# Kernel tuning notes

Hardware: AMD Instinct MI355X
Metric: run time of the kernel (lower is better)

The kernel has to match this reference:

```python
import jax, jax.numpy as jnp
import numpy as np
import math

B, T, D = 2, 2048, 1024
H, DH = 16, 64  # n_heads, d_head
ROPE_THETA = 10000.0


def _rope_cos_sin(seq_len, d_head, dtype):
    # inv_freq over even indices, freqs[i,j] = t_i * inv_freq_j, shape [T, d_head//2]
    inv_freq = 1.0 / (ROPE_THETA ** (jnp.arange(0, d_head, 2, dtype=jnp.float32) / d_head))
    freqs = jnp.arange(seq_len, dtype=jnp.float32)[:, None] * inv_freq[None, :]
    # emb = cat(freqs, freqs); we only ever index cos[..., :d_head//2], so keep the half
    cos = jnp.cos(freqs).astype(dtype)[None, :, None, :]  # [1,T,1,DH/2]
    sin = jnp.sin(freqs).astype(dtype)[None, :, None, :]
    return cos, sin


def _apply_rotation(x, cos, sin):
    # x: [B,T,H,DH]; rotate-half style as in the torch module
    x1, x2 = x[..., : x.shape[-1] // 2], x[..., x.shape[-1] // 2 :]
    return jnp.concatenate([x1 * cos - x2 * sin, x1 * sin + x2 * cos], axis=-1)


def setup_inputs() -> dict:
    key = jax.random.key(0)
    k1, k2, k3 = jax.random.split(key, 3)
    x = jax.random.normal(k1, (B, T, D), dtype=jnp.float32)
    # torch Linear weights stored transposed here as [in, out]; init_std=0.02
    Wqkv = jax.random.normal(k2, (D, 3 * D), dtype=jnp.float32) * 0.02
    Wout = jax.random.normal(k3, (D, D), dtype=jnp.float32) * 0.02
    return {"x": x, "Wqkv": Wqkv, "Wout": Wout}


def reference(x, Wqkv, Wout):
    b, t, d = x.shape
    qkv = x @ Wqkv  # [B,T,3D]
    q, k, v = jnp.split(qkv, 3, axis=-1)
    q = q.reshape(b, t, H, DH)
    k = k.reshape(b, t, H, DH)
    v = v.reshape(b, t, H, DH)

    cos, sin = _rope_cos_sin(t, DH, x.dtype)
    q = _apply_rotation(q, cos, sin)
    k = _apply_rotation(k, cos, sin)

    scale = 1.0 / math.sqrt(DH)
    # scores: [B,H,Tq,Tk]
    scores = jnp.einsum("bqhd,bkhd->bhqk", q, k) * scale
    causal = jnp.triu(jnp.ones((t, t), dtype=bool), k=1)
    scores = jnp.where(causal[None, None, :, :], -jnp.inf, scores)
    attn = jax.nn.softmax(scores, axis=-1)
    # dropout in eval mode -> identity
    out = jnp.einsum("bhqk,bkhd->bqhd", attn, v).reshape(b, t, d)
    return out @ Wout
```

## Files before the change

### kernel.cpp

```cpp
#include <hip/hip_runtime.h>
#include <hip/hip_bf16.h>
#include <stdint.h>
#include <math.h>

#define T_SEQ 2048
#define NHEAD 16
#define NBH   32
#define BTROW 4096

typedef __bf16 bf16_t;
typedef __bf16 bf16x4_t __attribute__((ext_vector_type(4)));
typedef __bf16 bf16x8_t __attribute__((ext_vector_type(8)));
typedef float  f32x4_t  __attribute__((ext_vector_type(4)));

#define QSCALE 0.18033688011112042f

__device__ __forceinline__ f32x4_t mfma16(bf16x8_t a, bf16x8_t b, f32x4_t c) {
  return __builtin_amdgcn_mfma_f32_16x16x32_bf16(a, b, c, 0, 0, 0);
}

__device__ __forceinline__ float fast_exp2(float x) {
#if __has_builtin(__builtin_amdgcn_exp2f)
  return __builtin_amdgcn_exp2f(x);
#else
  return exp2f(x);
#endif
}

__device__ __forceinline__ void gl_lds16(const bf16_t* g, bf16_t* l) {
  __builtin_amdgcn_global_load_lds(
      (const __attribute__((address_space(1))) void*)g,
      (__attribute__((address_space(3))) void*)l, 16, 0, 0);
}

__global__ __launch_bounds__(256) void k_cast_bf16(const float* __restrict__ in,
                                                   bf16_t* __restrict__ out, int n) {
  int tid = blockIdx.x * blockDim.x + threadIdx.x;
  int stride = gridDim.x * blockDim.x;
  for (int i = tid * 4; i < n; i += stride * 4) {
    float4 a = *(const float4*)(in + i);
    bf16x4_t r = { (bf16_t)a.x, (bf16_t)a.y, (bf16_t)a.z, (bf16_t)a.w };
    *(bf16x4_t*)(out + i) = r;
  }
}

__global__ __launch_bounds__(256) void k_trans_cast(const float* __restrict__ W,
                                                    bf16_t* __restrict__ WT,
                                                    int K, int N) {
  __shared__ float tile[32][33];
  int n0 = blockIdx.x * 32, k0 = blockIdx.y * 32;
  int tx = threadIdx.x & 31, ty = threadIdx.x >> 5;
#pragma unroll
  for (int j = 0; j < 4; j++)
    tile[ty + j * 8][tx] = W[(size_t)(k0 + ty + j * 8) * N + n0 + tx];
  __syncthreads();
#pragma unroll
  for (int j = 0; j < 4; j++)
    WT[(size_t)(n0 + ty + j * 8) * K + k0 + tx] = (bf16_t)tile[tx][ty + j * 8];
}

__global__ __launch_bounds__(256) void k_rope_table(float* __restrict__ cs,
                                                    float* __restrict__ sn) {
  int i = blockIdx.x * blockDim.x + threadIdx.x;
  if (i >= T_SEQ * 32) return;
  int t = i >> 5, j = i & 31;
  float inv = powf(10000.0f, -(float)(2 * j) / 64.0f);
  float f = (float)t * inv;
  cs[i] = cosf(f);
  sn[i] = sinf(f);
}

__global__ __launch_bounds__(256) void k_gemm_qkv(const bf16_t* __restrict__ A,
                                                  const bf16_t* __restrict__ Bt,
                                                  const float* __restrict__ cs,
                                                  const float* __restrict__ sn,
                                                  bf16_t* __restrict__ Qr,
                                                  bf16_t* __restrict__ Kr,
                                                  bf16_t* __restrict__ Vt) {
  const int K = 1024;
  __shared__ __align__(16) unsigned char smem[33792];
  bf16_t* vtile = (bf16_t*)smem;

  int m0 = blockIdx.y * 128, n0 = blockIdx.x * 128;
  int tid = threadIdx.x;
  int lane = tid & 63, w = tid >> 6;
  int wr = w >> 1, wc = w & 1;
  int l15 = lane & 15, l4 = lane >> 4;

  f32x4_t acc[4][4];
#pragma unroll
  for (int m = 0; m < 4; m++)
#pragma unroll
    for (int n = 0; n < 4; n++) acc[m][n] = (f32x4_t){0.f, 0.f, 0.f, 0.f};

  auto stageg = [&](int bf, int k0) {
    bf16_t* As = (bf16_t*)(smem + bf * 16384);
    bf16_t* Bs = (bf16_t*)(smem + 8192 + bf * 16384);
#pragma unroll
    for (int j = 0; j < 2; j++) {
      int c = j * 256 + tid;
      int row = c >> 2, kb = c & 3;
      gl_lds16(A + (size_t)(m0 + row) * K + k0 + kb * 8, As + (size_t)(j * 256 + w * 64) * 8);
      gl_lds16(Bt + (size_t)(n0 + row) * K + k0 + kb * 8, Bs + (size_t)(j * 256 + w * 64) * 8);
    }
  };

  stageg(0, 0);
  for (int kt = 0; kt < 32; kt++) {
    int cb = kt & 1;
    bf16_t* As = (bf16_t*)(smem + cb * 16384);
    bf16_t* Bs = (bf16_t*)(smem + 8192 + cb * 16384);
    asm volatile("s_waitcnt vmcnt(0)" ::: "memory");
    __builtin_amdgcn_s_barrier();
    if (kt + 1 < 32) stageg(cb ^ 1, (kt + 1) * 32);
    bf16x8_t af[4], bfr[4];
#pragma unroll
    for (int m = 0; m < 4; m++)
      af[m] = *(const bf16x8_t*)(As + (size_t)(wr * 64 + m * 16 + l15) * 32 + l4 * 8);
#pragma unroll
    for (int n = 0; n < 4; n++)
      bfr[n] = *(const bf16x8_t*)(Bs + (size_t)(wc * 64 + n * 16 + l15) * 32 + l4 * 8);
#pragma unroll
    for (int m = 0; m < 4; m++)
#pragma unroll
      for (int n = 0; n < 4; n++) acc[m][n] = mfma16(af[m], bfr[n], acc[m][n]);
  }
  __syncthreads();

  int region = n0 >> 10;
  if (region < 2) {
    bf16_t* dst = region ? Kr : Qr;
    float qs = region ? 1.0f : QSCALE;
    int h = ((n0 & 1023) + wc * 64) >> 6;
#pragma unroll
    for (int m = 0; m < 4; m++)
#pragma unroll
      for (int r = 0; r < 4; r++) {
        int row = m0 + wr * 64 + m * 16 + l4 * 4 + r;
        int b = row >> 11, t = row & 2047;
        size_t obase = ((size_t)(b * NHEAD + h) * T_SEQ + t) * 64;
#pragma unroll
        for (int n = 0; n < 2; n++) {
          int j = n * 16 + l15;
          float c = cs[t * 32 + j], s = sn[t * 32 + j];
          float x1 = acc[m][n][r], x2 = acc[m][n + 2][r];
          dst[obase + j]      = (bf16_t)((x1 * c - x2 * s) * qs);
          dst[obase + 32 + j] = (bf16_t)((x1 * s + x2 * c) * qs);
        }
      }
  } else {
#pragma unroll
    for (int m = 0; m < 4; m++)
#pragma unroll
      for (int n = 0; n < 4; n++)
#pragma unroll
        for (int r = 0; r < 4; r++)
          vtile[(size_t)(wc * 64 + n * 16 + l15) * 132 + wr * 64 + m * 16 + l4 * 4 + r] =
              (bf16_t)acc[m][n][r];
    __syncthreads();
    int colbase = n0 - 2048;
    int b = m0 >> 11, t0l = m0 & 2047;
#pragma unroll
    for (int p = 0; p < 64; p++) {
      int idx = p * 256 + tid;
      int dl = idx >> 7, tl = idx & 127;
      int col = colbase + dl, h = col >> 6, d = col & 63;
      Vt[((size_t)(b * NHEAD + h) * 64 + d) * T_SEQ + t0l + tl] = vtile[(size_t)dl * 132 + tl];
    }
  }
}

__global__ __launch_bounds__(256) void k_gemm2(const bf16_t* __restrict__ A,
                                               const bf16_t* __restrict__ Bt,
                                               float* __restrict__ C) {
  const int N = 1024, K = 1024;
  __shared__ __align__(16) bf16_t As[2][64 * 32];
  __shared__ __align__(16) bf16_t Bs[2][128 * 32];
  int m0 = blockIdx.y * 64, n0 = blockIdx.x * 128;
  int tid = threadIdx.x;
  int lane = tid & 63, w = tid >> 6;
  int l15 = lane & 15, l4 = lane >> 4;

  f32x4_t acc[4][2];
#pragma unroll
  for (int m = 0; m < 4; m++)
#pragma unroll
    for (int n = 0; n < 2; n++) acc[m][n] = (f32x4_t){0.f, 0.f, 0.f, 0.f};

  auto stageg = [&](int bf, int k0) {
    {
      int row = tid >> 2, kb = tid & 3;
      gl_lds16(A + (size_t)(m0 + row) * K + k0 + kb * 8, &As[bf][0] + (size_t)(w * 64) * 8);
    }
#pragma unroll
    for (int j = 0; j < 2; j++) {
      int c = j * 256 + tid;
      int row = c >> 2, kb = c & 3;
      gl_lds16(Bt + (size_t)(n0 + row) * K + k0 + kb * 8, &Bs[bf][0] + (size_t)(j * 256 + w * 64) * 8);
    }
  };

  stageg(0, 0);
  for (int kt = 0; kt < 32; kt++) {
    int cb = kt & 1;
    asm volatile("s_waitcnt vmcnt(0)" ::: "memory");
    __builtin_amdgcn_s_barrier();
    if (kt + 1 < 32) stageg(cb ^ 1, (kt + 1) * 32);
    bf16x8_t af[4], bfr[2];
#pragma unroll
    for (int m = 0; m < 4; m++)
      af[m] = *(const bf16x8_t*)(&As[cb][0] + (size_t)(m * 16 + l15) * 32 + l4 * 8);
#pragma unroll
    for (int n = 0; n < 2; n++)
      bfr[n] = *(const bf16x8_t*)(&Bs[cb][0] + (size_t)(w * 32 + n * 16 + l15) * 32 + l4 * 8);
#pragma unroll
    for (int m = 0; m < 4; m++)
#pragma unroll
      for (int n = 0; n < 2; n++) acc[m][n] = mfma16(af[m], bfr[n], acc[m][n]);
  }
#pragma unroll
  for (int m = 0; m < 4; m++)
#pragma unroll
    for (int n = 0; n < 2; n++)
#pragma unroll
      for (int r = 0; r < 4; r++) {
        int row = m0 + m * 16 + l4 * 4 + r;
        int col = n0 + w * 32 + n * 16 + l15;
        C[(size_t)row * N + col] = acc[m][n][r];
      }
}

__global__ __launch_bounds__(512, 4) void k_attn(const bf16_t* __restrict__ Qr,
                                                 const bf16_t* __restrict__ Kr,
                                                 const bf16_t* __restrict__ Vt,
                                                 bf16_t* __restrict__ Ob) {
  __shared__ __align__(16) bf16_t Ks[2][2][64 * 64];
  __shared__ __align__(16) bf16_t Vs[2][2][64 * 64];
  __shared__ __align__(16) bf16_t Ps[8][16 * 64];
  int flat = blockIdx.x;
  int swz = (flat & 7) * 64 + (flat >> 3);
  int pair = swz & 15, bh = swz >> 4;
  int b = bh >> 4, h = bh & 15;
  int tid = threadIdx.x, lane = tid & 63, w = tid >> 6;
  int grp = w >> 2, wl = w & 3;
  int l15 = lane & 15, l4 = lane >> 4;

  const bf16_t* Kbh = Kr + (size_t)bh * T_SEQ * 64;
  const bf16_t* Vbh = Vt + (size_t)bh * 64 * T_SEQ;

  int srow = tid >> 3;
  int sk8 = (tid & 7) ^ (srow & 7);

  auto stage = [&](int buf, int i) {
#pragma unroll
    for (int tp = 0; tp < 2; tp++) {
      int kb = (2 * i + tp) * 64;
      gl_lds16(Kbh + (size_t)(kb + srow) * 64 + sk8 * 8, &Ks[buf][tp][0] + (size_t)w * 512);
      gl_lds16(Vbh + (size_t)srow * T_SEQ + kb + sk8 * 8, &Vs[buf][tp][0] + (size_t)w * 512);
    }
  };

  char* myPs = (char*)&Ps[w][0];

  bf16x8_t ones;
#pragma unroll
  for (int i = 0; i < 8; i++) ones[i] = (bf16_t)1.0f;

  for (int pass = 0; pass < 2; pass++) {
    int qb = pass ? (31 - pair) : pair;
    int q0 = qb * 64;
    int niter = (qb + 2) >> 1;

    bf16x8_t qf[2];
    size_t qbase = ((size_t)bh * T_SEQ + q0 + wl * 16 + l15) * 64;
    qf[0] = *(const bf16x8_t*)(Qr + qbase + l4 * 8);
    qf[1] = *(const bf16x8_t*)(Qr + qbase + 32 + l4 * 8);

    f32x4_t o[4];
#pragma unroll
    for (int n = 0; n < 4; n++) o[n] = (f32x4_t){0.f, 0.f, 0.f, 0.f};
    f32x4_t ls = (f32x4_t){0.f, 0.f, 0.f, 0.f};
    float m_s = -1e30f;

    stage(0, 0);

    for (int i = 0; i < niter; i++) {
      int cur = i & 1;
      asm volatile("s_waitcnt vmcnt(0)" ::: "memory");
      __builtin_amdgcn_s_barrier();
      if (i + 1 < niter) stage(cur ^ 1, i + 1);

      int t = 2 * i + grp;
      if (t <= qb) {
        const bf16_t* Kt = &Ks[cur][grp][0];
        const bf16_t* Vtl = &Vs[cur][grp][0];

        f32x4_t s[4];
        __builtin_amdgcn_s_setprio(1);
#pragma unroll
        for (int n = 0; n < 4; n++) {
          int rowK = n * 16 + l15;
          const bf16_t* kp = Kt + (size_t)rowK * 64;
          int sw = rowK & 7;
          bf16x8_t kf0 = *(const bf16x8_t*)(kp + (l4 ^ sw) * 8);
          bf16x8_t kf1 = *(const bf16x8_t*)(kp + ((l4 ^ 4) ^ sw) * 8);
          s[n] = (f32x4_t){0.f, 0.f, 0.f, 0.f};
          s[n] = mfma16(kf0, qf[0], s[n]);
          s[n] = mfma16(kf1, qf[1], s[n]);
        }
        __builtin_amdgcn_s_setprio(0);

        if (t == qb) {
#pragma unroll
          for (int n = 0; n < 4; n++)
#pragma unroll
            for (int r = 0; r < 4; r++)
              if (n * 16 + l4 * 4 + r > wl * 16 + l15) s[n][r] = -1e30f;
        }

        float t0 = fmaxf(fmaxf(s[0][0], s[0][1]), fmaxf(s[0][2], s[0][3]));
        float t1 = fmaxf(fmaxf(s[1][0], s[1][1]), fmaxf(s[1][2], s[1][3]));
        float t2 = fmaxf(fmaxf(s[2][0], s[2][1]), fmaxf(s[2][2], s[2][3]));
        float t3 = fmaxf(fmaxf(s[3][0], s[3][1]), fmaxf(s[3][2], s[3][3]));
        float mx = fmaxf(fmaxf(t0, t1), fmaxf(t2, t3));
        mx = fmaxf(mx, __shfl_xor(mx, 16, 64));
        mx = fmaxf(mx, __shfl_xor(mx, 32, 64));

        if (__any(mx - m_s > 8.0f)) {
          float mnew = fmaxf(m_s, mx);
          float alpha = fast_exp2(m_s - mnew);
          m_s = mnew;
          float ar[4];
#pragma unroll
          for (int r = 0; r < 4; r++) ar[r] = __shfl(alpha, l4 * 4 + r, 64);
#pragma unroll
          for (int n = 0; n < 4; n++)
#pragma unroll
            for (int r = 0; r < 4; r++) o[n][r] *= ar[r];
#pragma unroll
          for (int r = 0; r < 4; r++) ls[r] *= ar[r];
        }

#pragma unroll
        for (int n = 0; n < 4; n++) {
#pragma unroll
          for (int r = 0; r < 4; r++) s[n][r] = fast_exp2(s[n][r] - m_s);
          bf16x4_t pk = { (bf16_t)s[n][0], (bf16_t)s[n][1], (bf16_t)s[n][2], (bf16_t)s[n][3] };
          *(bf16x4_t*)(myPs + l15 * 128 +
                       ((((n << 1) | (l4 >> 1)) ^ (l15 & 7)) << 4) + ((l4 & 1) << 3)) = pk;
        }

        __builtin_amdgcn_s_setprio(1);
#pragma unroll
        for (int ks = 0; ks < 2; ks++) {
          bf16x8_t pa = *(const bf16x8_t*)(myPs + l15 * 128 +
                                           ((((ks << 2) | l4) ^ (l15 & 7)) << 4));
          ls = mfma16(pa, ones, ls);
#pragma unroll
          for (int n = 0; n < 4; n++) {
            int rowV = n * 16 + l15;
            bf16x8_t vf = *(const bf16x8_t*)(Vtl + (size_t)rowV * 64 +
                                             (((ks * 4 + l4) ^ (rowV & 7)) * 8));
            o[n] = mfma16(pa, vf, o[n]);
          }
        }
        __builtin_amdgcn_s_setprio(0);
      }
    }

    __syncthreads();
    float* mg = (float*)&Ks[0][0][0];
    int base = (wl * 64 + lane) * 25;
    if (grp == 1) {
#pragma unroll
      for (int n = 0; n < 4; n++)
#pragma unroll
        for (int r = 0; r < 4; r++) mg[base + n * 4 + r] = o[n][r];
#pragma unroll
      for (int r = 0; r < 4; r++) mg[base + 16 + r] = ls[r];
#pragma unroll
      for (int r = 0; r < 4; r++) mg[base + 20 + r] = __shfl(m_s, l4 * 4 + r, 64);
    }
    __syncthreads();
    if (grp == 0) {
#pragma unroll
      for (int r = 0; r < 4; r++) {
        float mA = __shfl(m_s, l4 * 4 + r, 64);
        float mB = mg[base + 20 + r];
        float mF = fmaxf(mA, mB);
        float fA = fast_exp2(mA - mF), fB = fast_exp2(mB - mF);
        float lF = ls[r] * fA + mg[base + 16 + r] * fB;
        float ir = 1.0f / lF;
        int q = q0 + wl * 16 + l4 * 4 + r;
        size_t off = ((size_t)(b * T_SEQ + q)) * 1024 + h * 64;
#pragma unroll
        for (int n = 0; n < 4; n++) {
          float val = o[n][r] * fA + mg[base + n * 4 + r] * fB;
          Ob[off + n * 16 + l15] = (bf16_t)(val * ir);
        }
      }
    }
    __syncthreads();
  }
}

extern "C" void kernel_launch(void* const* d_in, const int* in_sizes, int n_in,
                              void* d_out, int out_size, void* d_ws, size_t ws_size,
                              hipStream_t stream) {
  const float* x    = (const float*)d_in[0];
  const float* Wqkv = (const float*)d_in[1];
  const float* Wout = (const float*)d_in[2];
  float* out = (float*)d_out;
  char* ws = (char*)d_ws;

  bf16_t* wqkvT = (bf16_t*)(ws + 0);
  bf16_t* woutT = (bf16_t*)(ws + 6291456);
  bf16_t* xb    = (bf16_t*)(ws + 8388608);
  bf16_t* Qr    = (bf16_t*)(ws + 41943040);
  bf16_t* Kr    = (bf16_t*)(ws + 50331648);
  bf16_t* Vt    = (bf16_t*)(ws + 58720256);
  float*  cs    = (float*)(ws + 67108864);
  float*  sn    = (float*)(ws + 67371008);
  bf16_t* Ob    = xb;

  k_cast_bf16<<<2048, 256, 0, stream>>>(x, xb, 4096 * 1024);
  k_trans_cast<<<dim3(3072 / 32, 1024 / 32), 256, 0, stream>>>(Wqkv, wqkvT, 1024, 3072);
  k_trans_cast<<<dim3(1024 / 32, 1024 / 32), 256, 0, stream>>>(Wout, woutT, 1024, 1024);
  k_rope_table<<<(T_SEQ * 32) / 256, 256, 0, stream>>>(cs, sn);

  k_gemm_qkv<<<dim3(3072 / 128, 4096 / 128), 256, 0, stream>>>(xb, wqkvT, cs, sn, Qr, Kr, Vt);
  k_attn<<<512, 512, 0, stream>>>(Qr, Kr, Vt, Ob);
  k_gemm2<<<dim3(1024 / 128, 4096 / 64), 256, 0, stream>>>(Ob, woutT, out);
}
```

Measured before the change: 119.1 us.

## Fuse x cast into QKV GEMM and hoist V fragment loads in attention

Removes the standalone fp32-to-bf16 cast kernel: the QKV GEMM now stages fp32 x tiles into LDS with an XOR swizzle and converts to bf16 when building MFMA fragments. This saves one launch and the write and re-read of the bf16 copy of x. The cost is double the A-tile LDS footprint and global traffic per tile, plus conversion work inside the K loop. In attention, all V fragments are loaded before the softmax to hide LDS latency, and the cross-lane max reduction now runs only when a rescale is triggered.

```diff
diff --git a/kernel.cpp b/kernel.cpp
--- a/kernel.cpp
+++ b/kernel.cpp
@@ -32,16 +32,10 @@
       (const __attribute__((address_space(1))) void*)g,
       (__attribute__((address_space(3))) void*)l, 16, 0, 0);
 }
-
-__global__ __launch_bounds__(256) void k_cast_bf16(const float* __restrict__ in,
-                                                   bf16_t* __restrict__ out, int n) {
-  int tid = blockIdx.x * blockDim.x + threadIdx.x;
-  int stride = gridDim.x * blockDim.x;
-  for (int i = tid * 4; i < n; i += stride * 4) {
-    float4 a = *(const float4*)(in + i);
-    bf16x4_t r = { (bf16_t)a.x, (bf16_t)a.y, (bf16_t)a.z, (bf16_t)a.w };
-    *(bf16x4_t*)(out + i) = r;
-  }
+__device__ __forceinline__ void gl_lds16f(const float* g, float* l) {
+  __builtin_amdgcn_global_load_lds(
+      (const __attribute__((address_space(1))) void*)g,
+      (__attribute__((address_space(3))) void*)l, 16, 0, 0);
 }
 
 __global__ __launch_bounds__(256) void k_trans_cast(const float* __restrict__ W,
@@ -70,7 +64,7 @@
   sn[i] = sinf(f);
 }
 
-__global__ __launch_bounds__(256) void k_gemm_qkv(const bf16_t* __restrict__ A,
+__global__ __launch_bounds__(256) void k_gemm_qkv(const float* __restrict__ A,
                                                   const bf16_t* __restrict__ Bt,
                                                   const float* __restrict__ cs,
                                                   const float* __restrict__ sn,
@@ -78,7 +72,7 @@
                                                   bf16_t* __restrict__ Kr,
                                                   bf16_t* __restrict__ Vt) {
   const int K = 1024;
-  __shared__ __align__(16) unsigned char smem[33792];
+  __shared__ __align__(16) unsigned char smem[49152];
   bf16_t* vtile = (bf16_t*)smem;
 
   int m0 = blockIdx.y * 128, n0 = blockIdx.x * 128;
@@ -94,13 +88,19 @@
     for (int n = 0; n < 4; n++) acc[m][n] = (f32x4_t){0.f, 0.f, 0.f, 0.f};
 
   auto stageg = [&](int bf, int k0) {
-    bf16_t* As = (bf16_t*)(smem + bf * 16384);
-    bf16_t* Bs = (bf16_t*)(smem + 8192 + bf * 16384);
+    float* Asf = (float*)(smem + bf * 24576);
+    bf16_t* Bs = (bf16_t*)(smem + 16384 + bf * 24576);
+#pragma unroll
+    for (int j = 0; j < 4; j++) {
+      int c = j * 256 + tid;
+      int row = c >> 3, g = c & 7;
+      int gs = g ^ (row & 7);
+      gl_lds16f(A + (size_t)(m0 + row) * K + k0 + gs * 4, Asf + (size_t)(j * 256 + w * 64) * 4);
+    }
 #pragma unroll
     for (int j = 0; j < 2; j++) {
       int c = j * 256 + tid;
       int row = c >> 2, kb = c & 3;
-      gl_lds16(A + (size_t)(m0 + row) * K + k0 + kb * 8, As + (size_t)(j * 256 + w * 64) * 8);
       gl_lds16(Bt + (size_t)(n0 + row) * K + k0 + kb * 8, Bs + (size_t)(j * 256 + w * 64) * 8);
     }
   };
@@ -108,15 +108,26 @@
   stageg(0, 0);
   for (int kt = 0; kt < 32; kt++) {
     int cb = kt & 1;
-    bf16_t* As = (bf16_t*)(smem + cb * 16384);
-    bf16_t* Bs = (bf16_t*)(smem + 8192 + cb * 16384);
+    float* Asf = (float*)(smem + cb * 24576);
+    bf16_t* Bs = (bf16_t*)(smem + 16384 + cb * 24576);
     asm volatile("s_waitcnt vmcnt(0)" ::: "memory");
     __builtin_amdgcn_s_barrier();
     if (kt + 1 < 32) stageg(cb ^ 1, (kt + 1) * 32);
+
     bf16x8_t af[4], bfr[4];
 #pragma unroll
-    for (int m = 0; m < 4; m++)
-      af[m] = *(const bf16x8_t*)(As + (size_t)(wr * 64 + m * 16 + l15) * 32 + l4 * 8);
+    for (int m = 0; m < 4; m++) {
+      int rowA = wr * 64 + m * 16 + l15;
+      int sw = rowA & 7;
+      const float* ap = Asf + (size_t)rowA * 32;
+      int g0 = (2 * l4) ^ sw;
+      float4 ra = *(const float4*)(ap + g0 * 4);
+      float4 rb = *(const float4*)(ap + (g0 ^ 1) * 4);
+      bf16x8_t t;
+      t[0] = (bf16_t)ra.x; t[1] = (bf16_t)ra.y; t[2] = (bf16_t)ra.z; t[3] = (bf16_t)ra.w;
+      t[4] = (bf16_t)rb.x; t[5] = (bf16_t)rb.y; t[6] = (bf16_t)rb.z; t[7] = (bf16_t)rb.w;
+      af[m] = t;
+    }
 #pragma unroll
     for (int n = 0; n < 4; n++)
       bfr[n] = *(const bf16x8_t*)(Bs + (size_t)(wc * 64 + n * 16 + l15) * 32 + l4 * 8);
@@ -310,6 +321,16 @@
         }
         __builtin_amdgcn_s_setprio(0);
 
+        bf16x8_t vfr[8];
+#pragma unroll
+        for (int ks = 0; ks < 2; ks++)
+#pragma unroll
+          for (int n = 0; n < 4; n++) {
+            int rowV = n * 16 + l15;
+            vfr[ks * 4 + n] = *(const bf16x8_t*)(Vtl + (size_t)rowV * 64 +
+                                                 (((ks * 4 + l4) ^ (rowV & 7)) * 8));
+          }
+
         if (t == qb) {
 #pragma unroll
           for (int n = 0; n < 4; n++)
@@ -322,11 +343,11 @@
         float t1 = fmaxf(fmaxf(s[1][0], s[1][1]), fmaxf(s[1][2], s[1][3]));
         float t2 = fmaxf(fmaxf(s[2][0], s[2][1]), fmaxf(s[2][2], s[2][3]));
         float t3 = fmaxf(fmaxf(s[3][0], s[3][1]), fmaxf(s[3][2], s[3][3]));
-        float mx = fmaxf(fmaxf(t0, t1), fmaxf(t2, t3));
-        mx = fmaxf(mx, __shfl_xor(mx, 16, 64));
-        mx = fmaxf(mx, __shfl_xor(mx, 32, 64));
-
-        if (__any(mx - m_s > 8.0f)) {
+        float mloc = fmaxf(fmaxf(t0, t1), fmaxf(t2, t3));
+
+        if (__any(mloc - m_s > 8.0f)) {
+          float mx = fmaxf(mloc, __shfl_xor(mloc, 16, 64));
+          mx = fmaxf(mx, __shfl_xor(mx, 32, 64));
           float mnew = fmaxf(m_s, mx);
           float alpha = fast_exp2(m_s - mnew);
           m_s = mnew;
@@ -357,12 +378,7 @@
                                            ((((ks << 2) | l4) ^ (l15 & 7)) << 4));
           ls = mfma16(pa, ones, ls);
 #pragma unroll
-          for (int n = 0; n < 4; n++) {
-            int rowV = n * 16 + l15;
-            bf16x8_t vf = *(const bf16x8_t*)(Vtl + (size_t)rowV * 64 +
-                                             (((ks * 4 + l4) ^ (rowV & 7)) * 8));
-            o[n] = mfma16(pa, vf, o[n]);
-          }
+          for (int n = 0; n < 4; n++) o[n] = mfma16(pa, vfr[ks * 4 + n], o[n]);
         }
         __builtin_amdgcn_s_setprio(0);
       }
@@ -415,20 +431,18 @@
 
   bf16_t* wqkvT = (bf16_t*)(ws + 0);
   bf16_t* woutT = (bf16_t*)(ws + 6291456);
-  bf16_t* xb    = (bf16_t*)(ws + 8388608);
+  bf16_t* Ob    = (bf16_t*)(ws + 8388608);
   bf16_t* Qr    = (bf16_t*)(ws + 41943040);
   bf16_t* Kr    = (bf16_t*)(ws + 50331648);
   bf16_t* Vt    = (bf16_t*)(ws + 58720256);
   float*  cs    = (float*)(ws + 67108864);
   float*  sn    = (float*)(ws + 67371008);
-  bf16_t* Ob    = xb;
-
-  k_cast_bf16<<<2048, 256, 0, stream>>>(x, xb, 4096 * 1024);
+
   k_trans_cast<<<dim3(3072 / 32, 1024 / 32), 256, 0, stream>>>(Wqkv, wqkvT, 1024, 3072);
   k_trans_cast<<<dim3(1024 / 32, 1024 / 32), 256, 0, stream>>>(Wout, woutT, 1024, 1024);
   k_rope_table<<<(T_SEQ * 32) / 256, 256, 0, stream>>>(cs, sn);
 
-  k_gemm_qkv<<<dim3(3072 / 128, 4096 / 128), 256, 0, stream>>>(xb, wqkvT, cs, sn, Qr, Kr, Vt);
+  k_gemm_qkv<<<dim3(3072 / 128, 4096 / 128), 256, 0, stream>>>(x, wqkvT, cs, sn, Qr, Kr, Vt);
   k_attn<<<512, 512, 0, stream>>>(Qr, Kr, Vt, Ob);
   k_gemm2<<<dim3(1024 / 128, 4096 / 64), 256, 0, stream>>>(Ob, woutT, out);
 }
```

After: 119.7 us. Within noise of the previous version (+0.6%).
